# Optimization experiments

Measured on AMD Instinct MI355X. Metric: run time of the kernel, lower is better.

## Reference

```python
import jax, jax.numpy as jnp
import numpy as np

H = 256
W = 256
CHUNK = 100  # faces per rasterizer scan step


def _cross2(o, p, q):
    # 2D cross product of (p-o) x (q-o); broadcasts over leading dims
    return (p[..., 0] - o[..., 0]) * (q[..., 1] - o[..., 1]) - (p[..., 1] - o[..., 1]) * (q[..., 0] - o[..., 0])


def transform(verts, K, Rt):
    # verts [B,V,3] -> pixel coords [B,V,3] = (x_pix, y_pix, z_cam)
    v_cam = jnp.einsum('bij,bnj->bni', Rt[:, :, :3], verts) + Rt[:, None, :, 3]
    v_proj = jnp.einsum('bij,bnj->bni', K, v_cam)
    z = v_cam[..., 2:3]
    return jnp.concatenate([v_proj[..., :2] / z, z], axis=-1)


def _pixel_centers(h, w, dtype):
    px = jnp.arange(w, dtype=dtype) + 0.5
    py = jnp.arange(h, dtype=dtype) + 0.5
    gx, gy = jnp.meshgrid(px, py, indexing='xy')  # [h,w]
    return gx, gy


def rasterize(v_pix, vi, h, w):
    # z-buffered triangle rasterization -> index image [B,h,w] (int32, -1 = bg)
    B = v_pix.shape[0]
    Fc = vi.shape[0]
    gx, gy = _pixel_centers(h, w, v_pix.dtype)
    pix = jnp.stack([gx.ravel(), gy.ravel()], axis=-1)  # [HW,2]
    face_ids = jnp.arange(Fc, dtype=jnp.int32).reshape(-1, CHUNK)
    inf = jnp.asarray(jnp.inf, v_pix.dtype)

    def step(carry, fids):
        best_z, best_i = carry
        tri = vi[fids]                      # [C,3]
        p = v_pix[:, tri]                   # [B,C,3,3]
        a, b, c = p[:, :, 0], p[:, :, 1], p[:, :, 2]
        area = _cross2(a[..., :2], b[..., :2], c[..., :2])  # [B,C]
        pixb = pix[None, None]              # [1,1,HW,2]
        w0 = _cross2(b[..., None, :2], c[..., None, :2], pixb)  # [B,C,HW]
        w1 = _cross2(c[..., None, :2], a[..., None, :2], pixb)
        w2 = _cross2(a[..., None, :2], b[..., None, :2], pixb)
        s = jnp.sign(area)[..., None]
        nz = jnp.abs(area)[..., None] > 1e-8
        inside = (w0 * s >= 0) & (w1 * s >= 0) & (w2 * s >= 0) & nz
        za, zb, zc = a[..., 2:3], b[..., 2:3], c[..., 2:3]
        valid = inside & (za > 0) & (zb > 0) & (zc > 0)
        ar = jnp.where(jnp.abs(area) > 1e-8, area, 1.0)[..., None]
        invz = (w0 / ar) / za + (w1 / ar) / zb + (w2 / ar) / zc  # persp-correct 1/z
        z = jnp.where(valid & (invz > 0), 1.0 / jnp.maximum(invz, 1e-12), inf)
        cz = z.min(axis=1)                  # [B,HW]
        ci = z.argmin(axis=1)
        cf = fids[ci]
        upd = cz < best_z
        return (jnp.where(upd, cz, best_z), jnp.where(upd, cf, best_i)), None

    init = (jnp.full((B, h * w), jnp.inf, v_pix.dtype), jnp.full((B, h * w), -1, jnp.int32))
    (_, bi), _ = jax.lax.scan(step, init, face_ids)
    return bi.reshape(B, h, w)


def render(v_pix, vi, index_img):
    # depth [B,h,w] and perspective-correct barycentrics [B,3,h,w]
    B, h, w = index_img.shape
    tri = vi[jnp.clip(index_img, 0)]                 # [B,h,w,3]
    p = jax.vmap(lambda v, t: v[t])(v_pix, tri)      # [B,h,w,3,3]
    gx, gy = _pixel_centers(h, w, v_pix.dtype)
    pt = jnp.stack([gx, gy], axis=-1)[None]          # [1,h,w,2]
    a, b, c = p[..., 0, :], p[..., 1, :], p[..., 2, :]
    w0 = _cross2(b[..., :2], c[..., :2], pt)
    w1 = _cross2(c[..., :2], a[..., :2], pt)
    w2 = _cross2(a[..., :2], b[..., :2], pt)
    area = w0 + w1 + w2
    ar = jnp.where(jnp.abs(area) > 1e-8, area, 1.0)
    f0 = (w0 / ar) / jnp.maximum(a[..., 2], 1e-8)
    f1 = (w1 / ar) / jnp.maximum(b[..., 2], 1e-8)
    f2 = (w2 / ar) / jnp.maximum(c[..., 2], 1e-8)
    invz = f0 + f1 + f2
    invz_s = jnp.where(jnp.abs(invz) > 1e-12, invz, 1.0)
    depth = 1.0 / invz_s
    bary = jnp.stack([f0, f1, f2], axis=-1) / invz_s[..., None]  # [B,h,w,3]
    m = index_img != -1
    depth_img = jnp.where(m, depth, 0.0)
    bary_img = jnp.where(m[..., None], bary, 0.0).transpose(0, 3, 1, 2)  # [B,3,h,w]
    return depth_img, bary_img


def interpolate(attr, vti, index_img, bary_img):
    # attr [B,N,D], bary_img [B,3,h,w] -> [B,D,h,w]
    tri = vti[jnp.clip(index_img, 0)]                # [B,h,w,3]
    av = jax.vmap(lambda a, t: a[t])(attr, tri)      # [B,h,w,3,D]
    return jnp.einsum('bhwkd,bkhw->bdhw', av, bary_img)


def grid_sample_bilinear(tex, grid):
    # tex [B,C,Ht,Wt], grid [B,h,w,2] in [-1,1]; align_corners=False, zero pad
    B, C, Ht, Wt = tex.shape
    x = (grid[..., 0] + 1.0) * Wt / 2.0 - 0.5
    y = (grid[..., 1] + 1.0) * Ht / 2.0 - 0.5
    x0 = jnp.floor(x)
    y0 = jnp.floor(y)
    wx = (x - x0)[:, None]
    wy = (y - y0)[:, None]
    x0i = x0.astype(jnp.int32)
    y0i = y0.astype(jnp.int32)

    def gat(ix, iy):
        valid = (ix >= 0) & (ix < Wt) & (iy >= 0) & (iy < Ht)
        ixc = jnp.clip(ix, 0, Wt - 1)
        iyc = jnp.clip(iy, 0, Ht - 1)
        v = jax.vmap(lambda t, yy, xx: t[:, yy, xx])(tex, iyc, ixc)  # [B,C,h,w]
        return v * valid[:, None].astype(tex.dtype)

    return (gat(x0i, y0i) * (1 - wx) * (1 - wy)
            + gat(x0i + 1, y0i) * wx * (1 - wy)
            + gat(x0i, y0i + 1) * (1 - wx) * wy
            + gat(x0i + 1, y0i + 1) * wx * wy)


def reference(verts, tex, K, Rt, vt, vi, vti):
    v_pix = transform(verts, K, Rt)
    index_img = jax.lax.stop_gradient(rasterize(v_pix, vi, H, W))
    depth_img, bary_img = render(v_pix, vi, index_img)
    B = verts.shape[0]
    vt_attr = jnp.broadcast_to((vt * 2.0 - 1.0)[None], (B,) + vt.shape)
    vt_img = interpolate(vt_attr, vti, index_img, bary_img)    # [B,2,H,W]
    mask = (index_img != -1)[:, None].astype(tex.dtype)
    img = grid_sample_bilinear(tex, vt_img.transpose(0, 2, 3, 1)) * mask
    # edge_grad_estimator is identity in the forward pass
    return img, depth_img, v_pix, vt_img, index_img, bary_img, mask


def setup_inputs() -> dict:
    key = jax.random.key(0)
    ks = jax.random.split(key, 6)
    B, V, Fc, Nvt = 2, 5000, 10000, 5000
    xy = jax.random.uniform(ks[0], (B, V, 2), minval=-1.5, maxval=1.5)
    z = jax.random.uniform(ks[1], (B, V, 1), minval=2.0, maxval=4.0)
    verts = jnp.concatenate([xy, z], axis=-1)
    tex = jax.random.uniform(ks[2], (B, 3, 1024, 1024), dtype=jnp.float32)
    K = jnp.broadcast_to(jnp.array([[256., 0., 128.], [0., 256., 128.], [0., 0., 1.]], dtype=jnp.float32), (B, 3, 3))
    Rt = jnp.broadcast_to(jnp.concatenate([jnp.eye(3, dtype=jnp.float32), jnp.zeros((3, 1), jnp.float32)], axis=1), (B, 3, 4))
    vt = jax.random.uniform(ks[3], (Nvt, 2), dtype=jnp.float32)
    vi = jax.random.randint(ks[4], (Fc, 3), 0, V).astype(jnp.int32)
    vti = jax.random.randint(ks[5], (Fc, 3), 0, Nvt).astype(jnp.int32)
    return {"verts": verts, "tex": tex, "K": K, "Rt": Rt, "vt": vt, "vi": vi, "vti": vti}
```

## Files before the change

### kernel.cpp

```cpp
#include <hip/hip_runtime.h>
#include <cmath>

#define H_ 256
#define W_ 256
#define NB 256
#define BANDSH 3
#define NBAND (H_ >> BANDSH)
#define ILV 4
#define INITKEY 0x7f800000FFFFFFFFull

__device__ inline unsigned fkey(float f) {
  unsigned u = __float_as_uint(f);
  return (u & 0x80000000u) ? ~u : (u | 0x80000000u);
}
__device__ inline float unfkey(unsigned k) {
  return (k & 0x80000000u) ? __uint_as_float(k & 0x7fffffffu) : __uint_as_float(~k);
}

__device__ inline int zbucket(float zmin, float zlo, float scale) {
  int bkt = 0;
  if (zmin == zmin) bkt = min(NB - 1, max(0, (int)((zmin - zlo) * scale)));
  return bkt;
}

__global__ void k_transform(const float* __restrict__ verts, const float* __restrict__ Km,
                            const float* __restrict__ Rt, float* __restrict__ vpix,
                            int B, int V) {
  int i = blockIdx.x * blockDim.x + threadIdx.x;
  if (i >= B * V) return;
  int b = i / V;
  float x = verts[(size_t)i * 3 + 0], y = verts[(size_t)i * 3 + 1], z = verts[(size_t)i * 3 + 2];
  const float* R = Rt + (size_t)b * 12;
  float cx = __fadd_rn(__fadd_rn(__fadd_rn(__fmul_rn(R[0], x), __fmul_rn(R[1], y)), __fmul_rn(R[2], z)), R[3]);
  float cy = __fadd_rn(__fadd_rn(__fadd_rn(__fmul_rn(R[4], x), __fmul_rn(R[5], y)), __fmul_rn(R[6], z)), R[7]);
  float cz = __fadd_rn(__fadd_rn(__fadd_rn(__fmul_rn(R[8], x), __fmul_rn(R[9], y)), __fmul_rn(R[10], z)), R[11]);
  const float* Kb = Km + (size_t)b * 9;
  float px = __fadd_rn(__fadd_rn(__fmul_rn(Kb[0], cx), __fmul_rn(Kb[1], cy)), __fmul_rn(Kb[2], cz));
  float py = __fadd_rn(__fadd_rn(__fmul_rn(Kb[3], cx), __fmul_rn(Kb[4], cy)), __fmul_rn(Kb[5], cz));
  vpix[(size_t)i * 3 + 0] = __fdiv_rn(px, cz);
  vpix[(size_t)i * 3 + 1] = __fdiv_rn(py, cz);
  vpix[(size_t)i * 3 + 2] = cz;
}

__global__ void k_init(int* __restrict__ cnt, int* __restrict__ bcur, int n,
                       unsigned* __restrict__ minmax) {
  int i = blockIdx.x * blockDim.x + threadIdx.x;
  if (i < n) { cnt[i] = 0; bcur[i] = 0; }
  if (i == 0) { minmax[0] = 0xFFFFFFFFu; minmax[1] = 0u; }
}

__global__ void k_faceprep(const float* __restrict__ vpix, const int* __restrict__ vi,
                           float4* __restrict__ sA, float4* __restrict__ sB4,
                           float4* __restrict__ sC, float4* __restrict__ sZ1,
                           float4* __restrict__ meta, unsigned* __restrict__ minmax,
                           int B, int V, int F) {
  int i = blockIdx.x * blockDim.x + threadIdx.x;
  unsigned kmin = 0xFFFFFFFFu, kmax = 0u;
  if (i < B * F) {
    int b = i / F, f = i - b * F;
    int i0 = vi[f * 3 + 0], i1 = vi[f * 3 + 1], i2 = vi[f * 3 + 2];
    const float* base = vpix + (size_t)b * V * 3;
    float ax = base[(size_t)i0 * 3], ay = base[(size_t)i0 * 3 + 1], az = base[(size_t)i0 * 3 + 2];
    float bx = base[(size_t)i1 * 3], by = base[(size_t)i1 * 3 + 1], bz = base[(size_t)i1 * 3 + 2];
    float cx = base[(size_t)i2 * 3], cy = base[(size_t)i2 * 3 + 1], cz = base[(size_t)i2 * 3 + 2];
    float e0x = __fsub_rn(cx, bx), e0y = __fsub_rn(cy, by);
    float e1x = __fsub_rn(ax, cx), e1y = __fsub_rn(ay, cy);
    float e2x = __fsub_rn(bx, ax), e2y = __fsub_rn(by, ay);
    float area = __fsub_rn(__fmul_rn(e2x, __fsub_rn(cy, ay)), __fmul_rn(e2y, __fsub_rn(cx, ax)));
    float s = (area > 0.f) ? 1.f : ((area < 0.f) ? -1.f : 0.f);
    bool nz = fabsf(area) > 1e-8f;
    bool zv = (az > 0.f) && (bz > 0.f) && (cz > 0.f);
    float sp = (nz && zv) ? s : __uint_as_float(0x7fc00000u);
    float ar = nz ? area : 1.0f;
    float zmin = fminf(az, fminf(bz, cz));
    sA[i]  = make_float4(ax, ay, bx, by);
    sB4[i] = make_float4(cx, cy, __fmul_rn(sp, e0x), __fmul_rn(sp, e0y));
    sC[i]  = make_float4(__fmul_rn(sp, e1x), __fmul_rn(sp, e1y),
                         __fmul_rn(sp, e2x), __fmul_rn(sp, e2y));
    sZ1[i] = make_float4(az, bz, cz, __fmul_rn(sp, ar));
    unsigned bbox = 0x00000001u;
    if (sp == sp) {
      float minx = fminf(ax, fminf(bx, cx)), maxx = fmaxf(ax, fmaxf(bx, cx));
      float miny = fminf(ay, fminf(by, cy)), maxy = fmaxf(ay, fmaxf(by, cy));
      int xl = (int)ceilf(fmaxf(fminf(minx - 0.5f, 1e9f), -1e9f));
      int xh = (int)floorf(fmaxf(fminf(maxx - 0.5f, 1e9f), -1e9f));
      int yl = (int)ceilf(fmaxf(fminf(miny - 0.5f, 1e9f), -1e9f));
      int yh = (int)floorf(fmaxf(fminf(maxy - 0.5f, 1e9f), -1e9f));
      if (!(xl > xh || yl > yh || xh < 0 || xl > W_ - 1 || yh < 0 || yl > H_ - 1)) {
        int xlo = max(xl, 0), xhi = min(xh, W_ - 1);
        int ylo = max(yl, 0), yhi = min(yh, H_ - 1);
        bbox = (unsigned)xlo | ((unsigned)xhi << 8) | ((unsigned)ylo << 16) | ((unsigned)yhi << 24);
      }
    }
    meta[i] = make_float4(zmin, __uint_as_float(bbox), 0.f, 0.f);
    if (zmin == zmin) { kmin = fkey(zmin); kmax = kmin; }
  }
  #pragma unroll
  for (int m = 32; m >= 1; m >>= 1) {
    kmin = min(kmin, (unsigned)__shfl_xor((int)kmin, m));
    kmax = max(kmax, (unsigned)__shfl_xor((int)kmax, m));
  }
  if ((threadIdx.x & 63) == 0) {
    atomicMin(&minmax[0], kmin);
    atomicMax(&minmax[1], kmax);
  }
}

__global__ void k_hist(const float4* __restrict__ meta, const unsigned* __restrict__ minmax,
                       int* __restrict__ cnt, int B, int F) {
  int i = blockIdx.x * blockDim.x + threadIdx.x;
  if (i >= B * F) return;
  int b = i / F;
  float4 m = meta[i];
  unsigned bbox = __float_as_uint(m.y);
  int xlo = (int)(bbox & 255u), xhi = (int)((bbox >> 8) & 255u);
  if (xlo > xhi) return;
  float zlo = unfkey(minmax[0]), zhi = unfkey(minmax[1]);
  float scale = (float)NB / fmaxf(zhi - zlo, 1e-12f);
  int bkt = zbucket(m.x, zlo, scale);
  int ylo = (int)((bbox >> 16) & 255u), yhi = (int)(bbox >> 24);
  for (int band = (ylo >> BANDSH); band <= (yhi >> BANDSH); ++band)
    atomicAdd(&cnt[(b * NBAND + band) * NB + bkt], 1);
}

__global__ void k_bandscan(const int* __restrict__ cnt, int* __restrict__ bstart) {
  __shared__ int sh[NB];
  int rowi = blockIdx.x;
  int t = threadIdx.x;
  sh[t] = cnt[rowi * NB + t];
  __syncthreads();
  int self = sh[t];
  for (int ofs = 1; ofs < NB; ofs <<= 1) {
    int u = (t >= ofs) ? sh[t - ofs] : 0;
    __syncthreads();
    sh[t] += u;
    __syncthreads();
  }
  bstart[rowi * (NB + 1) + t] = sh[t] - self;
  if (t == NB - 1) bstart[rowi * (NB + 1) + NB] = sh[t];
}

__global__ void k_scatter(const float4* __restrict__ meta, const unsigned* __restrict__ minmax,
                          const int* __restrict__ bstart, int* __restrict__ bcur,
                          uint4* __restrict__ list, int B, int F) {
  int i = blockIdx.x * blockDim.x + threadIdx.x;
  if (i >= B * F) return;
  int b = i / F, f = i - b * F;
  float4 m = meta[i];
  unsigned bbox = __float_as_uint(m.y);
  int xlo = (int)(bbox & 255u), xhi = (int)((bbox >> 8) & 255u);
  if (xlo > xhi) return;
  float zlo = unfkey(minmax[0]), zhi = unfkey(minmax[1]);
  float rng = fmaxf(zhi - zlo, 1e-12f);
  float scale = (float)NB / rng;
  int bkt = zbucket(m.x, zlo, scale);
  float floorval = zlo + (float)bkt * (rng / (float)NB);
  uint4 ent = make_uint4(bbox, (unsigned)f, __float_as_uint(m.x), __float_as_uint(floorval));
  int ylo = (int)((bbox >> 16) & 255u), yhi = (int)(bbox >> 24);
  for (int band = (ylo >> BANDSH); band <= (yhi >> BANDSH); ++band) {
    int rowi = b * NBAND + band;
    int slot = bstart[rowi * (NB + 1) + bkt] + atomicAdd(&bcur[rowi * NB + bkt], 1);
    list[(size_t)rowi * F + slot] = ent;
  }
}

__global__ __launch_bounds__(64 * ILV) void k_raster_band(const uint4* __restrict__ list,
                                                          const int* __restrict__ bstart,
                                                          const float4* __restrict__ sA,
                                                          const float4* __restrict__ sB4,
                                                          const float4* __restrict__ sC,
                                                          const float4* __restrict__ sZ1,
                                                          float* __restrict__ o_idx,
                                                          int B, int F) {
  int seg = blockIdx.x;
  int y   = blockIdx.y;
  int b   = blockIdx.z;
  int tid = threadIdx.x;
  int w = tid >> 6, lane = tid & 63;
  __shared__ unsigned long long sk[64];
  if (tid < 64) sk[tid] = INITKEY;
  __syncthreads();
  int rowi = b * NBAND + (y >> BANDSH);
  int len = bstart[rowi * (NB + 1) + NB];
  const uint4* L = list + (size_t)rowi * F;
  size_t fb = (size_t)b * F;
  float px = seg * 64 + lane + 0.5f, py = y + 0.5f;
  int sx0 = seg * 64, sx1 = sx0 + 63;
  unsigned long long bestkey = INITKEY;
  float bestz = INFINITY;
  int it = 0;
  int pos = w;
  uint4 e = (pos < len) ? L[pos] : make_uint4(0x00000001u, 0u, 0u, 0x7f800000u);
  while (pos < len) {
    int nxt = pos + ILV;
    uint4 en = L[(nxt < len) ? nxt : (len - 1)];
    float floor0 = __fmul_rn(__uint_as_float(e.w), 0.9999f) - 1e-5f;
    if (__all(floor0 > bestz)) break;
    ++it;
    if ((it & 7) == 0) {
      unsigned long long old = atomicMin(&sk[lane], bestkey);
      if (old < bestkey) { bestkey = old; bestz = __uint_as_float((unsigned)(bestkey >> 32)); }
    }
    int xlo = (int)(e.x & 255u), xhi = (int)((e.x >> 8) & 255u);
    int ylo = (int)((e.x >> 16) & 255u), yhi = (int)(e.x >> 24);
    bool cull = (y < ylo) || (y > yhi) || (xhi < sx0) || (xlo > sx1);
    if (!cull) {
      int f = (int)e.y;
      float4 a0 = sA[fb + f];
      float4 a1 = sB4[fb + f];
      float4 a2 = sC[fb + f];
      float t0 = __fsub_rn(__fmul_rn(a1.z, __fsub_rn(py, a0.w)), __fmul_rn(a1.w, __fsub_rn(px, a0.z)));
      float t1 = __fsub_rn(__fmul_rn(a2.x, __fsub_rn(py, a1.y)), __fmul_rn(a2.y, __fsub_rn(px, a1.x)));
      float t2 = __fsub_rn(__fmul_rn(a2.z, __fsub_rn(py, a0.y)), __fmul_rn(a2.w, __fsub_rn(px, a0.x)));
      bool inside = (t0 >= 0.f) && (t1 >= 0.f) && (t2 >= 0.f);
      if (inside && !(__fmul_rn(__uint_as_float(e.z), 0.9999f) > bestz)) {
        float4 zz = sZ1[fb + f];
        float u0 = __fdiv_rn(__fdiv_rn(t0, zz.w), zz.x);
        float u1 = __fdiv_rn(__fdiv_rn(t1, zz.w), zz.y);
        float u2 = __fdiv_rn(__fdiv_rn(t2, zz.w), zz.z);
        float invz = __fadd_rn(__fadd_rn(u0, u1), u2);
        if (invz > 0.f) {
          float z = __fdiv_rn(1.0f, fmaxf(invz, 1e-12f));
          unsigned long long ck = ((unsigned long long)__float_as_uint(z) << 32) | e.y;
          if (ck < bestkey) {
            bestkey = ck; bestz = z;
            atomicMin(&sk[lane], ck);
          }
        }
      }
    }
    pos = nxt;
    e = en;
  }
  atomicMin(&sk[lane], bestkey);
  __syncthreads();
  if (tid < 64) {
    unsigned long long k = sk[tid];
    unsigned zb = (unsigned)(k >> 32);
    o_idx[(size_t)b * (H_ * W_) + (size_t)y * W_ + seg * 64 + tid] =
        (zb >= 0x7f800000u) ? -1.0f : (float)(int)(unsigned)(k & 0xffffffffu);
  }
}

__global__ void k_raster_direct(const float* __restrict__ vpix, const int* __restrict__ vi,
                                float* __restrict__ idxout, int B, int V, int F) {
  int p = blockIdx.x * blockDim.x + threadIdx.x;
  if (p >= B * H_ * W_) return;
  int b = p / (H_ * W_); int pid = p - b * (H_ * W_);
  float px = (pid & (W_ - 1)) + 0.5f, py = (pid >> 8) + 0.5f;
  const float* base = vpix + (size_t)b * V * 3;
  float bestz = INFINITY; int besti = -1;
  for (int f = 0; f < F; ++f) {
    int i0 = vi[f * 3], i1 = vi[f * 3 + 1], i2 = vi[f * 3 + 2];
    float ax = base[(size_t)i0 * 3], ay = base[(size_t)i0 * 3 + 1], za = base[(size_t)i0 * 3 + 2];
    float bx = base[(size_t)i1 * 3], by = base[(size_t)i1 * 3 + 1], zb = base[(size_t)i1 * 3 + 2];
    float cx = base[(size_t)i2 * 3], cy = base[(size_t)i2 * 3 + 1], zc = base[(size_t)i2 * 3 + 2];
    float e0x = __fsub_rn(cx, bx), e0y = __fsub_rn(cy, by);
    float e1x = __fsub_rn(ax, cx), e1y = __fsub_rn(ay, cy);
    float e2x = __fsub_rn(bx, ax), e2y = __fsub_rn(by, ay);
    float area = __fsub_rn(__fmul_rn(e2x, __fsub_rn(cy, ay)), __fmul_rn(e2y, __fsub_rn(cx, ax)));
    float s = (area > 0.f) ? 1.f : ((area < 0.f) ? -1.f : 0.f);
    bool nz = fabsf(area) > 1e-8f;
    bool zv = (za > 0.f) && (zb > 0.f) && (zc > 0.f);
    float sp = (nz && zv) ? s : __uint_as_float(0x7fc00000u);
    float ar = nz ? area : 1.0f;
    float w0 = __fsub_rn(__fmul_rn(e0x, __fsub_rn(py, by)), __fmul_rn(e0y, __fsub_rn(px, bx)));
    float w1 = __fsub_rn(__fmul_rn(e1x, __fsub_rn(py, cy)), __fmul_rn(e1y, __fsub_rn(px, cx)));
    float w2 = __fsub_rn(__fmul_rn(e2x, __fsub_rn(py, ay)), __fmul_rn(e2y, __fsub_rn(px, ax)));
    bool inside = (__fmul_rn(w0, sp) >= 0.f) && (__fmul_rn(w1, sp) >= 0.f) && (__fmul_rn(w2, sp) >= 0.f);
    if (inside) {
      float invz = __fadd_rn(__fadd_rn(__fdiv_rn(__fdiv_rn(w0, ar), za),
                                       __fdiv_rn(__fdiv_rn(w1, ar), zb)),
                             __fdiv_rn(__fdiv_rn(w2, ar), zc));
      if (invz > 0.f) {
        float z = __fdiv_rn(1.0f, fmaxf(invz, 1e-12f));
        if (z < bestz) { bestz = z; besti = f; }
      }
    }
  }
  idxout[p] = (float)besti;
}

__global__ __launch_bounds__(256) void k_render(const float* __restrict__ vpix, const int* __restrict__ vi,
                                                const int* __restrict__ vti, const float* __restrict__ vt,
                                                const float* __restrict__ tex, const float* __restrict__ idxin,
                                                float* __restrict__ o_img, float* __restrict__ o_depth,
                                                float* __restrict__ o_vt, float* __restrict__ o_bary,
                                                float* __restrict__ o_mask,
                                                int B, int V, int F, int TH, int TW) {
  int p = blockIdx.x * blockDim.x + threadIdx.x;
  if (p >= B * H_ * W_) return;
  int HW = H_ * W_;
  int b = p / HW; int pid = p - b * HW;
  int y = pid >> 8, x = pid & (W_ - 1);
  int idx = (int)idxin[p];
  size_t pix2 = (size_t)b * 2 * HW + pid;
  size_t pix3 = (size_t)b * 3 * HW + pid;
  if (idx < 0) {
    o_depth[p] = 0.f; o_mask[p] = 0.f;
    o_vt[pix2] = 0.f; o_vt[pix2 + HW] = 0.f;
    o_bary[pix3] = 0.f; o_bary[pix3 + HW] = 0.f; o_bary[pix3 + 2 * HW] = 0.f;
    o_img[pix3] = 0.f; o_img[pix3 + HW] = 0.f; o_img[pix3 + 2 * HW] = 0.f;
    return;
  }
  const float* base = vpix + (size_t)b * V * 3;
  int i0 = vi[idx * 3], i1 = vi[idx * 3 + 1], i2 = vi[idx * 3 + 2];
  float ax = base[(size_t)i0 * 3], ay = base[(size_t)i0 * 3 + 1], az = base[(size_t)i0 * 3 + 2];
  float bx = base[(size_t)i1 * 3], by = base[(size_t)i1 * 3 + 1], bz = base[(size_t)i1 * 3 + 2];
  float cx = base[(size_t)i2 * 3], cy = base[(size_t)i2 * 3 + 1], cz = base[(size_t)i2 * 3 + 2];
  float ptx = x + 0.5f, pty = y + 0.5f;
  float w0 = __fsub_rn(__fmul_rn(__fsub_rn(cx, bx), __fsub_rn(pty, by)),
                       __fmul_rn(__fsub_rn(cy, by), __fsub_rn(ptx, bx)));
  float w1 = __fsub_rn(__fmul_rn(__fsub_rn(ax, cx), __fsub_rn(pty, cy)),
                       __fmul_rn(__fsub_rn(ay, cy), __fsub_rn(ptx, cx)));
  float w2 = __fsub_rn(__fmul_rn(__fsub_rn(bx, ax), __fsub_rn(pty, ay)),
                       __fmul_rn(__fsub_rn(by, ay), __fsub_rn(ptx, ax)));
  float area = __fadd_rn(__fadd_rn(w0, w1), w2);
  float ar = (fabsf(area) > 1e-8f) ? area : 1.0f;
  float f0 = __fdiv_rn(__fdiv_rn(w0, ar), fmaxf(az, 1e-8f));
  float f1 = __fdiv_rn(__fdiv_rn(w1, ar), fmaxf(bz, 1e-8f));
  float f2 = __fdiv_rn(__fdiv_rn(w2, ar), fmaxf(cz, 1e-8f));
  float invz = __fadd_rn(__fadd_rn(f0, f1), f2);
  float invz_s = (fabsf(invz) > 1e-12f) ? invz : 1.0f;
  float depth = __fdiv_rn(1.0f, invz_s);
  float bary0 = __fdiv_rn(f0, invz_s);
  float bary1 = __fdiv_rn(f1, invz_s);
  float bary2 = __fdiv_rn(f2, invz_s);
  o_depth[p] = depth; o_mask[p] = 1.0f;
  o_bary[pix3] = bary0; o_bary[pix3 + HW] = bary1; o_bary[pix3 + 2 * HW] = bary2;
  int t0 = vti[idx * 3], t1 = vti[idx * 3 + 1], t2 = vti[idx * 3 + 2];
  float u0x = __fsub_rn(__fmul_rn(vt[(size_t)t0 * 2], 2.f), 1.f);
  float u0y = __fsub_rn(__fmul_rn(vt[(size_t)t0 * 2 + 1], 2.f), 1.f);
  float u1x = __fsub_rn(__fmul_rn(vt[(size_t)t1 * 2], 2.f), 1.f);
  float u1y = __fsub_rn(__fmul_rn(vt[(size_t)t1 * 2 + 1], 2.f), 1.f);
  float u2x = __fsub_rn(__fmul_rn(vt[(size_t)t2 * 2], 2.f), 1.f);
  float u2y = __fsub_rn(__fmul_rn(vt[(size_t)t2 * 2 + 1], 2.f), 1.f);
  float gx = __fadd_rn(__fadd_rn(__fmul_rn(u0x, bary0), __fmul_rn(u1x, bary1)), __fmul_rn(u2x, bary2));
  float gy = __fadd_rn(__fadd_rn(__fmul_rn(u0y, bary0), __fmul_rn(u1y, bary1)), __fmul_rn(u2y, bary2));
  o_vt[pix2] = gx; o_vt[pix2 + HW] = gy;
  float sx = __fsub_rn(__fdiv_rn(__fmul_rn(__fadd_rn(gx, 1.0f), (float)TW), 2.0f), 0.5f);
  float sy = __fsub_rn(__fdiv_rn(__fmul_rn(__fadd_rn(gy, 1.0f), (float)TH), 2.0f), 0.5f);
  float x0f = floorf(sx), y0f = floorf(sy);
  float wx = __fsub_rn(sx, x0f), wy = __fsub_rn(sy, y0f);
  float omx = __fsub_rn(1.0f, wx), omy = __fsub_rn(1.0f, wy);
  int x0 = (int)x0f, y0 = (int)y0f;
  int x1 = x0 + 1, y1 = y0 + 1;
  bool v00 = (x0 >= 0) && (x0 < TW) && (y0 >= 0) && (y0 < TH);
  bool v10 = (x1 >= 0) && (x1 < TW) && (y0 >= 0) && (y0 < TH);
  bool v01 = (x0 >= 0) && (x0 < TW) && (y1 >= 0) && (y1 < TH);
  bool v11 = (x1 >= 0) && (x1 < TW) && (y1 >= 0) && (y1 < TH);
  int x0c = min(max(x0, 0), TW - 1), x1c = min(max(x1, 0), TW - 1);
  int y0c = min(max(y0, 0), TH - 1), y1c = min(max(y1, 0), TH - 1);
  const float* tb = tex + (size_t)b * 3 * TH * TW;
  #pragma unroll
  for (int ch = 0; ch < 3; ++ch) {
    const float* tc = tb + (size_t)ch * TH * TW;
    float g00 = v00 ? tc[(size_t)y0c * TW + x0c] : 0.f;
    float g10 = v10 ? tc[(size_t)y0c * TW + x1c] : 0.f;
    float g01 = v01 ? tc[(size_t)y1c * TW + x0c] : 0.f;
    float g11 = v11 ? tc[(size_t)y1c * TW + x1c] : 0.f;
    float r = __fmul_rn(__fmul_rn(g00, omx), omy);
    r = __fadd_rn(r, __fmul_rn(__fmul_rn(g10, wx), omy));
    r = __fadd_rn(r, __fmul_rn(__fmul_rn(g01, omx), wy));
    r = __fadd_rn(r, __fmul_rn(__fmul_rn(g11, wx), wy));
    o_img[pix3 + (size_t)ch * HW] = r;
  }
}

extern "C" void kernel_launch(void* const* d_in, const int* in_sizes, int n_in,
                              void* d_out, int out_size, void* d_ws, size_t ws_size,
                              hipStream_t stream) {
  const float* verts = (const float*)d_in[0];
  const float* tex   = (const float*)d_in[1];
  const float* Km    = (const float*)d_in[2];
  const float* Rt    = (const float*)d_in[3];
  const float* vt    = (const float*)d_in[4];
  const int*   vi    = (const int*)d_in[5];
  const int*   vti   = (const int*)d_in[6];

  int B = in_sizes[2] / 9;
  int V = in_sizes[0] / (3 * B);
  int F = in_sizes[5] / 3;
  long texhw = (long)in_sizes[1] / (B * 3);
  int TH = (int)(sqrt((double)texhw) + 0.5);
  int TW = TH;
  const int HW = H_ * W_;

  float* out = (float*)d_out;
  float* o_img   = out;
  float* o_depth = o_img + (size_t)B * 3 * HW;
  float* o_vpix  = o_depth + (size_t)B * HW;
  float* o_vt    = o_vpix + (size_t)B * V * 3;
  float* o_idx   = o_vt + (size_t)B * 2 * HW;
  float* o_bary  = o_idx + (size_t)B * HW;
  float* o_mask  = o_bary + (size_t)B * 3 * HW;

  k_transform<<<(B * V + 255) / 256, 256, 0, stream>>>(verts, Km, Rt, o_vpix, B, V);

  size_t f4Bytes   = (size_t)B * F * 16;
  size_t listBytes = (size_t)B * NBAND * F * 16;
  size_t cntBytes  = (size_t)B * NBAND * NB * 4;
  size_t bstBytes  = (size_t)B * NBAND * (NB + 1) * 4;
  size_t need = 5 * f4Bytes + listBytes + 2 * cntBytes + bstBytes + 64;

  if (ws_size >= need) {
    char* w = (char*)d_ws;
    float4* sA   = (float4*)w;  w += f4Bytes;
    float4* sB4  = (float4*)w;  w += f4Bytes;
    float4* sC   = (float4*)w;  w += f4Bytes;
    float4* sZ1  = (float4*)w;  w += f4Bytes;
    float4* meta = (float4*)w;  w += f4Bytes;
    uint4*  list = (uint4*)w;   w += listBytes;
    int*    cnt  = (int*)w;     w += cntBytes;
    int*    bcur = (int*)w;     w += cntBytes;
    int*    bst  = (int*)w;     w += bstBytes;
    unsigned* minmax = (unsigned*)w;

    int ninit = B * NBAND * NB;
    k_init<<<(ninit + 255) / 256, 256, 0, stream>>>(cnt, bcur, ninit, minmax);
    k_faceprep<<<(B * F + 255) / 256, 256, 0, stream>>>(o_vpix, vi, sA, sB4, sC, sZ1,
                                                        meta, minmax, B, V, F);
    k_hist<<<(B * F + 255) / 256, 256, 0, stream>>>(meta, minmax, cnt, B, F);
    k_bandscan<<<B * NBAND, NB, 0, stream>>>(cnt, bst);
    k_scatter<<<(B * F + 255) / 256, 256, 0, stream>>>(meta, minmax, bst, bcur, list, B, F);
    dim3 rg(W_ / 64, H_, B);
    k_raster_band<<<rg, 64 * ILV, 0, stream>>>(list, bst, sA, sB4, sC, sZ1, o_idx, B, F);
  } else {
    k_raster_direct<<<(B * HW + 255) / 256, 256, 0, stream>>>(o_vpix, vi, o_idx, B, V, F);
  }

  k_render<<<(B * HW + 255) / 256, 256, 0, stream>>>(o_vpix, vi, vti, vt, tex, o_idx,
                                                     o_img, o_depth, o_vt, o_bary, o_mask,
                                                     B, V, F, TH, TW);
}
```

Measured before the change: 380.6 us.

## Fuse z-range into transform, histogram into faceprep, add precomputed-record render

The depth range reduction moves into the vertex transform kernel, and the bucket histogram is folded into face preparation. This removes the separate histogram pass and the recomputation of buckets in scatter. The raster loop broadcasts list entries with readfirstlane and culls using a 64-pixel segment mask instead of a full x-bbox. A new render kernel reads per-face edge and UV records prepared in faceprep rather than re-gathering vertices, at the cost of four extra per-face float4 arrays of workspace. The z range is now taken over all vertices rather than face minima, which changes bucket boundaries.

```diff
diff --git a/kernel.cpp b/kernel.cpp
--- a/kernel.cpp
+++ b/kernel.cpp
@@ -25,21 +25,35 @@
 
 __global__ void k_transform(const float* __restrict__ verts, const float* __restrict__ Km,
                             const float* __restrict__ Rt, float* __restrict__ vpix,
-                            int B, int V) {
+                            unsigned* __restrict__ minmax, int B, int V) {
   int i = blockIdx.x * blockDim.x + threadIdx.x;
-  if (i >= B * V) return;
-  int b = i / V;
-  float x = verts[(size_t)i * 3 + 0], y = verts[(size_t)i * 3 + 1], z = verts[(size_t)i * 3 + 2];
-  const float* R = Rt + (size_t)b * 12;
-  float cx = __fadd_rn(__fadd_rn(__fadd_rn(__fmul_rn(R[0], x), __fmul_rn(R[1], y)), __fmul_rn(R[2], z)), R[3]);
-  float cy = __fadd_rn(__fadd_rn(__fadd_rn(__fmul_rn(R[4], x), __fmul_rn(R[5], y)), __fmul_rn(R[6], z)), R[7]);
-  float cz = __fadd_rn(__fadd_rn(__fadd_rn(__fmul_rn(R[8], x), __fmul_rn(R[9], y)), __fmul_rn(R[10], z)), R[11]);
-  const float* Kb = Km + (size_t)b * 9;
-  float px = __fadd_rn(__fadd_rn(__fmul_rn(Kb[0], cx), __fmul_rn(Kb[1], cy)), __fmul_rn(Kb[2], cz));
-  float py = __fadd_rn(__fadd_rn(__fmul_rn(Kb[3], cx), __fmul_rn(Kb[4], cy)), __fmul_rn(Kb[5], cz));
-  vpix[(size_t)i * 3 + 0] = __fdiv_rn(px, cz);
-  vpix[(size_t)i * 3 + 1] = __fdiv_rn(py, cz);
-  vpix[(size_t)i * 3 + 2] = cz;
+  unsigned kmin = 0xFFFFFFFFu, kmax = 0u;
+  if (i < B * V) {
+    int b = i / V;
+    float x = verts[(size_t)i * 3 + 0], y = verts[(size_t)i * 3 + 1], z = verts[(size_t)i * 3 + 2];
+    const float* R = Rt + (size_t)b * 12;
+    float cx = __fadd_rn(__fadd_rn(__fadd_rn(__fmul_rn(R[0], x), __fmul_rn(R[1], y)), __fmul_rn(R[2], z)), R[3]);
+    float cy = __fadd_rn(__fadd_rn(__fadd_rn(__fmul_rn(R[4], x), __fmul_rn(R[5], y)), __fmul_rn(R[6], z)), R[7]);
+    float cz = __fadd_rn(__fadd_rn(__fadd_rn(__fmul_rn(R[8], x), __fmul_rn(R[9], y)), __fmul_rn(R[10], z)), R[11]);
+    const float* Kb = Km + (size_t)b * 9;
+    float px = __fadd_rn(__fadd_rn(__fmul_rn(Kb[0], cx), __fmul_rn(Kb[1], cy)), __fmul_rn(Kb[2], cz));
+    float py = __fadd_rn(__fadd_rn(__fmul_rn(Kb[3], cx), __fmul_rn(Kb[4], cy)), __fmul_rn(Kb[5], cz));
+    vpix[(size_t)i * 3 + 0] = __fdiv_rn(px, cz);
+    vpix[(size_t)i * 3 + 1] = __fdiv_rn(py, cz);
+    vpix[(size_t)i * 3 + 2] = cz;
+    if (minmax && cz == cz) { kmin = fkey(cz); kmax = kmin; }
+  }
+  if (minmax) {
+    #pragma unroll
+    for (int m = 32; m >= 1; m >>= 1) {
+      kmin = min(kmin, (unsigned)__shfl_xor((int)kmin, m));
+      kmax = max(kmax, (unsigned)__shfl_xor((int)kmax, m));
+    }
+    if ((threadIdx.x & 63) == 0) {
+      atomicMin(&minmax[0], kmin);
+      atomicMax(&minmax[1], kmax);
+    }
+  }
 }
 
 __global__ void k_init(int* __restrict__ cnt, int* __restrict__ bcur, int n,
@@ -50,77 +64,71 @@
 }
 
 __global__ void k_faceprep(const float* __restrict__ vpix, const int* __restrict__ vi,
+                           const int* __restrict__ vti, const float* __restrict__ vt,
                            float4* __restrict__ sA, float4* __restrict__ sB4,
                            float4* __restrict__ sC, float4* __restrict__ sZ1,
-                           float4* __restrict__ meta, unsigned* __restrict__ minmax,
-                           int B, int V, int F) {
-  int i = blockIdx.x * blockDim.x + threadIdx.x;
-  unsigned kmin = 0xFFFFFFFFu, kmax = 0u;
-  if (i < B * F) {
-    int b = i / F, f = i - b * F;
-    int i0 = vi[f * 3 + 0], i1 = vi[f * 3 + 1], i2 = vi[f * 3 + 2];
-    const float* base = vpix + (size_t)b * V * 3;
-    float ax = base[(size_t)i0 * 3], ay = base[(size_t)i0 * 3 + 1], az = base[(size_t)i0 * 3 + 2];
-    float bx = base[(size_t)i1 * 3], by = base[(size_t)i1 * 3 + 1], bz = base[(size_t)i1 * 3 + 2];
-    float cx = base[(size_t)i2 * 3], cy = base[(size_t)i2 * 3 + 1], cz = base[(size_t)i2 * 3 + 2];
-    float e0x = __fsub_rn(cx, bx), e0y = __fsub_rn(cy, by);
-    float e1x = __fsub_rn(ax, cx), e1y = __fsub_rn(ay, cy);
-    float e2x = __fsub_rn(bx, ax), e2y = __fsub_rn(by, ay);
-    float area = __fsub_rn(__fmul_rn(e2x, __fsub_rn(cy, ay)), __fmul_rn(e2y, __fsub_rn(cx, ax)));
-    float s = (area > 0.f) ? 1.f : ((area < 0.f) ? -1.f : 0.f);
-    bool nz = fabsf(area) > 1e-8f;
-    bool zv = (az > 0.f) && (bz > 0.f) && (cz > 0.f);
-    float sp = (nz && zv) ? s : __uint_as_float(0x7fc00000u);
-    float ar = nz ? area : 1.0f;
-    float zmin = fminf(az, fminf(bz, cz));
-    sA[i]  = make_float4(ax, ay, bx, by);
-    sB4[i] = make_float4(cx, cy, __fmul_rn(sp, e0x), __fmul_rn(sp, e0y));
-    sC[i]  = make_float4(__fmul_rn(sp, e1x), __fmul_rn(sp, e1y),
-                         __fmul_rn(sp, e2x), __fmul_rn(sp, e2y));
-    sZ1[i] = make_float4(az, bz, cz, __fmul_rn(sp, ar));
-    unsigned bbox = 0x00000001u;
-    if (sp == sp) {
-      float minx = fminf(ax, fminf(bx, cx)), maxx = fmaxf(ax, fmaxf(bx, cx));
-      float miny = fminf(ay, fminf(by, cy)), maxy = fmaxf(ay, fmaxf(by, cy));
-      int xl = (int)ceilf(fmaxf(fminf(minx - 0.5f, 1e9f), -1e9f));
-      int xh = (int)floorf(fmaxf(fminf(maxx - 0.5f, 1e9f), -1e9f));
-      int yl = (int)ceilf(fmaxf(fminf(miny - 0.5f, 1e9f), -1e9f));
-      int yh = (int)floorf(fmaxf(fminf(maxy - 0.5f, 1e9f), -1e9f));
-      if (!(xl > xh || yl > yh || xh < 0 || xl > W_ - 1 || yh < 0 || yl > H_ - 1)) {
-        int xlo = max(xl, 0), xhi = min(xh, W_ - 1);
-        int ylo = max(yl, 0), yhi = min(yh, H_ - 1);
-        bbox = (unsigned)xlo | ((unsigned)xhi << 8) | ((unsigned)ylo << 16) | ((unsigned)yhi << 24);
-      }
-    }
-    meta[i] = make_float4(zmin, __uint_as_float(bbox), 0.f, 0.f);
-    if (zmin == zmin) { kmin = fkey(zmin); kmax = kmin; }
-  }
-  #pragma unroll
-  for (int m = 32; m >= 1; m >>= 1) {
-    kmin = min(kmin, (unsigned)__shfl_xor((int)kmin, m));
-    kmax = max(kmax, (unsigned)__shfl_xor((int)kmax, m));
-  }
-  if ((threadIdx.x & 63) == 0) {
-    atomicMin(&minmax[0], kmin);
-    atomicMax(&minmax[1], kmax);
-  }
-}
-
-__global__ void k_hist(const float4* __restrict__ meta, const unsigned* __restrict__ minmax,
-                       int* __restrict__ cnt, int B, int F) {
+                           float4* __restrict__ sE1, float4* __restrict__ sE2,
+                           float4* __restrict__ sUV12, float4* __restrict__ sUV2,
+                           float4* __restrict__ meta, const unsigned* __restrict__ minmax,
+                           int* __restrict__ cnt, int B, int V, int F) {
   int i = blockIdx.x * blockDim.x + threadIdx.x;
   if (i >= B * F) return;
-  int b = i / F;
-  float4 m = meta[i];
-  unsigned bbox = __float_as_uint(m.y);
-  int xlo = (int)(bbox & 255u), xhi = (int)((bbox >> 8) & 255u);
-  if (xlo > xhi) return;
+  int b = i / F, f = i - b * F;
+  int i0 = vi[f * 3 + 0], i1 = vi[f * 3 + 1], i2 = vi[f * 3 + 2];
+  const float* base = vpix + (size_t)b * V * 3;
+  float ax = base[(size_t)i0 * 3], ay = base[(size_t)i0 * 3 + 1], az = base[(size_t)i0 * 3 + 2];
+  float bx = base[(size_t)i1 * 3], by = base[(size_t)i1 * 3 + 1], bz = base[(size_t)i1 * 3 + 2];
+  float cx = base[(size_t)i2 * 3], cy = base[(size_t)i2 * 3 + 1], cz = base[(size_t)i2 * 3 + 2];
+  float e0x = __fsub_rn(cx, bx), e0y = __fsub_rn(cy, by);
+  float e1x = __fsub_rn(ax, cx), e1y = __fsub_rn(ay, cy);
+  float e2x = __fsub_rn(bx, ax), e2y = __fsub_rn(by, ay);
+  float area = __fsub_rn(__fmul_rn(e2x, __fsub_rn(cy, ay)), __fmul_rn(e2y, __fsub_rn(cx, ax)));
+  float s = (area > 0.f) ? 1.f : ((area < 0.f) ? -1.f : 0.f);
+  bool nz = fabsf(area) > 1e-8f;
+  bool zv = (az > 0.f) && (bz > 0.f) && (cz > 0.f);
+  float sp = (nz && zv) ? s : __uint_as_float(0x7fc00000u);
+  float ar = nz ? area : 1.0f;
+  float zmin = fminf(az, fminf(bz, cz));
+  sA[i]  = make_float4(ax, ay, bx, by);
+  sB4[i] = make_float4(cx, cy, __fmul_rn(sp, e0x), __fmul_rn(sp, e0y));
+  sC[i]  = make_float4(__fmul_rn(sp, e1x), __fmul_rn(sp, e1y),
+                       __fmul_rn(sp, e2x), __fmul_rn(sp, e2y));
+  sZ1[i] = make_float4(az, bz, cz, __fmul_rn(sp, ar));
+  sE1[i] = make_float4(cx, cy, e0x, e0y);
+  sE2[i] = make_float4(e1x, e1y, e2x, e2y);
+  int t0 = vti[f * 3], t1 = vti[f * 3 + 1], t2 = vti[f * 3 + 2];
+  float u0x = __fsub_rn(__fmul_rn(vt[(size_t)t0 * 2], 2.f), 1.f);
+  float u0y = __fsub_rn(__fmul_rn(vt[(size_t)t0 * 2 + 1], 2.f), 1.f);
+  float u1x = __fsub_rn(__fmul_rn(vt[(size_t)t1 * 2], 2.f), 1.f);
+  float u1y = __fsub_rn(__fmul_rn(vt[(size_t)t1 * 2 + 1], 2.f), 1.f);
+  float u2x = __fsub_rn(__fmul_rn(vt[(size_t)t2 * 2], 2.f), 1.f);
+  float u2y = __fsub_rn(__fmul_rn(vt[(size_t)t2 * 2 + 1], 2.f), 1.f);
+  sUV12[i] = make_float4(u0x, u0y, u1x, u1y);
+  sUV2[i]  = make_float4(u2x, u2y, 0.f, 0.f);
+  unsigned pack = 0u;
+  int bkt = 0; float floorval = 0.f;
   float zlo = unfkey(minmax[0]), zhi = unfkey(minmax[1]);
-  float scale = (float)NB / fmaxf(zhi - zlo, 1e-12f);
-  int bkt = zbucket(m.x, zlo, scale);
-  int ylo = (int)((bbox >> 16) & 255u), yhi = (int)(bbox >> 24);
-  for (int band = (ylo >> BANDSH); band <= (yhi >> BANDSH); ++band)
-    atomicAdd(&cnt[(b * NBAND + band) * NB + bkt], 1);
+  float rng = fmaxf(zhi - zlo, 1e-12f);
+  float scale = (float)NB / rng;
+  if (sp == sp) {
+    float minx = fminf(ax, fminf(bx, cx)), maxx = fmaxf(ax, fmaxf(bx, cx));
+    float miny = fminf(ay, fminf(by, cy)), maxy = fmaxf(ay, fmaxf(by, cy));
+    int xl = (int)ceilf(fmaxf(fminf(minx - 0.5f, 1e9f), -1e9f));
+    int xh = (int)floorf(fmaxf(fminf(maxx - 0.5f, 1e9f), -1e9f));
+    int yl = (int)ceilf(fmaxf(fminf(miny - 0.5f, 1e9f), -1e9f));
+    int yh = (int)floorf(fmaxf(fminf(maxy - 0.5f, 1e9f), -1e9f));
+    if (!(xl > xh || yl > yh || xh < 0 || xl > W_ - 1 || yh < 0 || yl > H_ - 1)) {
+      int xlo = max(xl, 0), xhi = min(xh, W_ - 1);
+      int ylo = max(yl, 0), yhi = min(yh, H_ - 1);
+      unsigned segmask = (((1u << ((xhi >> 6) + 1)) - 1u) & ~((1u << (xlo >> 6)) - 1u)) & 0xFu;
+      pack = segmask | ((unsigned)ylo << 8) | ((unsigned)yhi << 16);
+      bkt = zbucket(zmin, zlo, scale);
+      floorval = zlo + (float)bkt * (rng / (float)NB);
+      for (int band = (ylo >> BANDSH); band <= (yhi >> BANDSH); ++band)
+        atomicAdd(&cnt[(b * NBAND + band) * NB + bkt], 1);
+    }
+  }
+  meta[i] = make_float4(zmin, __uint_as_float(pack), __int_as_float(bkt), floorval);
 }
 
 __global__ void k_bandscan(const int* __restrict__ cnt, int* __restrict__ bstart) {
@@ -140,23 +148,18 @@
   if (t == NB - 1) bstart[rowi * (NB + 1) + NB] = sh[t];
 }
 
-__global__ void k_scatter(const float4* __restrict__ meta, const unsigned* __restrict__ minmax,
+__global__ void k_scatter(const float4* __restrict__ meta,
                           const int* __restrict__ bstart, int* __restrict__ bcur,
                           uint4* __restrict__ list, int B, int F) {
   int i = blockIdx.x * blockDim.x + threadIdx.x;
   if (i >= B * F) return;
   int b = i / F, f = i - b * F;
   float4 m = meta[i];
-  unsigned bbox = __float_as_uint(m.y);
-  int xlo = (int)(bbox & 255u), xhi = (int)((bbox >> 8) & 255u);
-  if (xlo > xhi) return;
-  float zlo = unfkey(minmax[0]), zhi = unfkey(minmax[1]);
-  float rng = fmaxf(zhi - zlo, 1e-12f);
-  float scale = (float)NB / rng;
-  int bkt = zbucket(m.x, zlo, scale);
-  float floorval = zlo + (float)bkt * (rng / (float)NB);
-  uint4 ent = make_uint4(bbox, (unsigned)f, __float_as_uint(m.x), __float_as_uint(floorval));
-  int ylo = (int)((bbox >> 16) & 255u), yhi = (int)(bbox >> 24);
+  unsigned pack = __float_as_uint(m.y);
+  if ((pack & 0xFu) == 0u) return;
+  int bkt = __float_as_int(m.z);
+  uint4 ent = make_uint4(pack, (unsigned)f, __float_as_uint(m.x), __float_as_uint(m.w));
+  int ylo = (int)((pack >> 8) & 255u), yhi = (int)((pack >> 16) & 255u);
   for (int band = (ylo >> BANDSH); band <= (yhi >> BANDSH); ++band) {
     int rowi = b * NBAND + band;
     int slot = bstart[rowi * (NB + 1) + bkt] + atomicAdd(&bcur[rowi * NB + bkt], 1);
@@ -185,43 +188,44 @@
   const uint4* L = list + (size_t)rowi * F;
   size_t fb = (size_t)b * F;
   float px = seg * 64 + lane + 0.5f, py = y + 0.5f;
-  int sx0 = seg * 64, sx1 = sx0 + 63;
   unsigned long long bestkey = INITKEY;
   float bestz = INFINITY;
   int it = 0;
   int pos = w;
-  uint4 e = (pos < len) ? L[pos] : make_uint4(0x00000001u, 0u, 0u, 0x7f800000u);
+  uint4 e = (pos < len) ? L[pos] : make_uint4(0u, 0u, 0u, 0x7f800000u);
   while (pos < len) {
     int nxt = pos + ILV;
     uint4 en = L[(nxt < len) ? nxt : (len - 1)];
-    float floor0 = __fmul_rn(__uint_as_float(e.w), 0.9999f) - 1e-5f;
+    unsigned pack = __builtin_amdgcn_readfirstlane(e.x);
+    int      fid  = __builtin_amdgcn_readfirstlane((int)e.y);
+    float    zmn  = __uint_as_float(__builtin_amdgcn_readfirstlane(e.z));
+    float    zfl  = __uint_as_float(__builtin_amdgcn_readfirstlane(e.w));
+    float floor0 = __fmul_rn(zfl, 0.9999f) - 1e-5f;
     if (__all(floor0 > bestz)) break;
     ++it;
     if ((it & 7) == 0) {
       unsigned long long old = atomicMin(&sk[lane], bestkey);
       if (old < bestkey) { bestkey = old; bestz = __uint_as_float((unsigned)(bestkey >> 32)); }
     }
-    int xlo = (int)(e.x & 255u), xhi = (int)((e.x >> 8) & 255u);
-    int ylo = (int)((e.x >> 16) & 255u), yhi = (int)(e.x >> 24);
-    bool cull = (y < ylo) || (y > yhi) || (xhi < sx0) || (xlo > sx1);
+    bool cull = !((pack >> seg) & 1u) ||
+                (y < (int)((pack >> 8) & 255u)) || (y > (int)((pack >> 16) & 255u));
     if (!cull) {
-      int f = (int)e.y;
-      float4 a0 = sA[fb + f];
-      float4 a1 = sB4[fb + f];
-      float4 a2 = sC[fb + f];
+      float4 a0 = sA[fb + fid];
+      float4 a1 = sB4[fb + fid];
+      float4 a2 = sC[fb + fid];
       float t0 = __fsub_rn(__fmul_rn(a1.z, __fsub_rn(py, a0.w)), __fmul_rn(a1.w, __fsub_rn(px, a0.z)));
       float t1 = __fsub_rn(__fmul_rn(a2.x, __fsub_rn(py, a1.y)), __fmul_rn(a2.y, __fsub_rn(px, a1.x)));
       float t2 = __fsub_rn(__fmul_rn(a2.z, __fsub_rn(py, a0.y)), __fmul_rn(a2.w, __fsub_rn(px, a0.x)));
       bool inside = (t0 >= 0.f) && (t1 >= 0.f) && (t2 >= 0.f);
-      if (inside && !(__fmul_rn(__uint_as_float(e.z), 0.9999f) > bestz)) {
-        float4 zz = sZ1[fb + f];
+      if (inside && !(__fmul_rn(zmn, 0.9999f) > bestz)) {
+        float4 zz = sZ1[fb + fid];
         float u0 = __fdiv_rn(__fdiv_rn(t0, zz.w), zz.x);
         float u1 = __fdiv_rn(__fdiv_rn(t1, zz.w), zz.y);
         float u2 = __fdiv_rn(__fdiv_rn(t2, zz.w), zz.z);
         float invz = __fadd_rn(__fadd_rn(u0, u1), u2);
         if (invz > 0.f) {
           float z = __fdiv_rn(1.0f, fmaxf(invz, 1e-12f));
-          unsigned long long ck = ((unsigned long long)__float_as_uint(z) << 32) | e.y;
+          unsigned long long ck = ((unsigned long long)__float_as_uint(z) << 32) | (unsigned)fid;
           if (ck < bestkey) {
             bestkey = ck; bestz = z;
             atomicMin(&sk[lane], ck);
@@ -279,6 +283,89 @@
     }
   }
   idxout[p] = (float)besti;
+}
+
+__global__ __launch_bounds__(256) void k_render_rec(const float4* __restrict__ sA,
+                                                    const float4* __restrict__ sE1,
+                                                    const float4* __restrict__ sE2,
+                                                    const float4* __restrict__ sZ1,
+                                                    const float4* __restrict__ sUV12,
+                                                    const float4* __restrict__ sUV2,
+                                                    const float* __restrict__ tex,
+                                                    const float* __restrict__ idxin,
+                                                    float* __restrict__ o_img, float* __restrict__ o_depth,
+                                                    float* __restrict__ o_vt, float* __restrict__ o_bary,
+                                                    float* __restrict__ o_mask,
+                                                    int B, int F, int TH, int TW) {
+  int p = blockIdx.x * blockDim.x + threadIdx.x;
+  if (p >= B * H_ * W_) return;
+  int HW = H_ * W_;
+  int b = p / HW; int pid = p - b * HW;
+  int y = pid >> 8, x = pid & (W_ - 1);
+  int idx = (int)idxin[p];
+  size_t pix2 = (size_t)b * 2 * HW + pid;
+  size_t pix3 = (size_t)b * 3 * HW + pid;
+  if (idx < 0) {
+    o_depth[p] = 0.f; o_mask[p] = 0.f;
+    o_vt[pix2] = 0.f; o_vt[pix2 + HW] = 0.f;
+    o_bary[pix3] = 0.f; o_bary[pix3 + HW] = 0.f; o_bary[pix3 + 2 * HW] = 0.f;
+    o_img[pix3] = 0.f; o_img[pix3 + HW] = 0.f; o_img[pix3 + 2 * HW] = 0.f;
+    return;
+  }
+  size_t gp = (size_t)b * F + idx;
+  float4 a0 = sA[gp];
+  float4 e1 = sE1[gp];
+  float4 e2 = sE2[gp];
+  float4 zz = sZ1[gp];
+  float4 uv = sUV12[gp];
+  float4 uv2 = sUV2[gp];
+  float ptx = x + 0.5f, pty = y + 0.5f;
+  float w0 = __fsub_rn(__fmul_rn(e1.z, __fsub_rn(pty, a0.w)), __fmul_rn(e1.w, __fsub_rn(ptx, a0.z)));
+  float w1 = __fsub_rn(__fmul_rn(e2.x, __fsub_rn(pty, e1.y)), __fmul_rn(e2.y, __fsub_rn(ptx, e1.x)));
+  float w2 = __fsub_rn(__fmul_rn(e2.z, __fsub_rn(pty, a0.y)), __fmul_rn(e2.w, __fsub_rn(ptx, a0.x)));
+  float area = __fadd_rn(__fadd_rn(w0, w1), w2);
+  float ar = (fabsf(area) > 1e-8f) ? area : 1.0f;
+  float f0 = __fdiv_rn(__fdiv_rn(w0, ar), fmaxf(zz.x, 1e-8f));
+  float f1 = __fdiv_rn(__fdiv_rn(w1, ar), fmaxf(zz.y, 1e-8f));
+  float f2 = __fdiv_rn(__fdiv_rn(w2, ar), fmaxf(zz.z, 1e-8f));
+  float invz = __fadd_rn(__fadd_rn(f0, f1), f2);
+  float invz_s = (fabsf(invz) > 1e-12f) ? invz : 1.0f;
+  float depth = __fdiv_rn(1.0f, invz_s);
+  float bary0 = __fdiv_rn(f0, invz_s);
+  float bary1 = __fdiv_rn(f1, invz_s);
+  float bary2 = __fdiv_rn(f2, invz_s);
+  o_depth[p] = depth; o_mask[p] = 1.0f;
+  o_bary[pix3] = bary0; o_bary[pix3 + HW] = bary1; o_bary[pix3 + 2 * HW] = bary2;
+  float gx = __fadd_rn(__fadd_rn(__fmul_rn(uv.x, bary0), __fmul_rn(uv.z, bary1)), __fmul_rn(uv2.x, bary2));
+  float gy = __fadd_rn(__fadd_rn(__fmul_rn(uv.y, bary0), __fmul_rn(uv.w, bary1)), __fmul_rn(uv2.y, bary2));
+  o_vt[pix2] = gx; o_vt[pix2 + HW] = gy;
+  float sx = __fsub_rn(__fdiv_rn(__fmul_rn(__fadd_rn(gx, 1.0f), (float)TW), 2.0f), 0.5f);
+  float sy = __fsub_rn(__fdiv_rn(__fmul_rn(__fadd_rn(gy, 1.0f), (float)TH), 2.0f), 0.5f);
+  float x0f = floorf(sx), y0f = floorf(sy);
+  float wx = __fsub_rn(sx, x0f), wy = __fsub_rn(sy, y0f);
+  float omx = __fsub_rn(1.0f, wx), omy = __fsub_rn(1.0f, wy);
+  int x0 = (int)x0f, y0 = (int)y0f;
+  int x1 = x0 + 1, y1 = y0 + 1;
+  bool v00 = (x0 >= 0) && (x0 < TW) && (y0 >= 0) && (y0 < TH);
+  bool v10 = (x1 >= 0) && (x1 < TW) && (y0 >= 0) && (y0 < TH);
+  bool v01 = (x0 >= 0) && (x0 < TW) && (y1 >= 0) && (y1 < TH);
+  bool v11 = (x1 >= 0) && (x1 < TW) && (y1 >= 0) && (y1 < TH);
+  int x0c = min(max(x0, 0), TW - 1), x1c = min(max(x1, 0), TW - 1);
+  int y0c = min(max(y0, 0), TH - 1), y1c = min(max(y1, 0), TH - 1);
+  const float* tb = tex + (size_t)b * 3 * TH * TW;
+  #pragma unroll
+  for (int ch = 0; ch < 3; ++ch) {
+    const float* tc = tb + (size_t)ch * TH * TW;
+    float g00 = v00 ? tc[(size_t)y0c * TW + x0c] : 0.f;
+    float g10 = v10 ? tc[(size_t)y0c * TW + x1c] : 0.f;
+    float g01 = v01 ? tc[(size_t)y1c * TW + x0c] : 0.f;
+    float g11 = v11 ? tc[(size_t)y1c * TW + x1c] : 0.f;
+    float r = __fmul_rn(__fmul_rn(g00, omx), omy);
+    r = __fadd_rn(r, __fmul_rn(__fmul_rn(g10, wx), omy));
+    r = __fadd_rn(r, __fmul_rn(__fmul_rn(g01, omx), wy));
+    r = __fadd_rn(r, __fmul_rn(__fmul_rn(g11, wx), wy));
+    o_img[pix3 + (size_t)ch * HW] = r;
+  }
 }
 
 __global__ __launch_bounds__(256) void k_render(const float* __restrict__ vpix, const int* __restrict__ vi,
@@ -395,41 +482,49 @@
   float* o_bary  = o_idx + (size_t)B * HW;
   float* o_mask  = o_bary + (size_t)B * 3 * HW;
 
-  k_transform<<<(B * V + 255) / 256, 256, 0, stream>>>(verts, Km, Rt, o_vpix, B, V);
-
   size_t f4Bytes   = (size_t)B * F * 16;
   size_t listBytes = (size_t)B * NBAND * F * 16;
   size_t cntBytes  = (size_t)B * NBAND * NB * 4;
   size_t bstBytes  = (size_t)B * NBAND * (NB + 1) * 4;
-  size_t need = 5 * f4Bytes + listBytes + 2 * cntBytes + bstBytes + 64;
+  size_t need = 9 * f4Bytes + listBytes + 2 * cntBytes + bstBytes + 64;
 
   if (ws_size >= need) {
     char* w = (char*)d_ws;
-    float4* sA   = (float4*)w;  w += f4Bytes;
-    float4* sB4  = (float4*)w;  w += f4Bytes;
-    float4* sC   = (float4*)w;  w += f4Bytes;
-    float4* sZ1  = (float4*)w;  w += f4Bytes;
-    float4* meta = (float4*)w;  w += f4Bytes;
-    uint4*  list = (uint4*)w;   w += listBytes;
-    int*    cnt  = (int*)w;     w += cntBytes;
-    int*    bcur = (int*)w;     w += cntBytes;
-    int*    bst  = (int*)w;     w += bstBytes;
+    float4* sA    = (float4*)w;  w += f4Bytes;
+    float4* sB4   = (float4*)w;  w += f4Bytes;
+    float4* sC    = (float4*)w;  w += f4Bytes;
+    float4* sZ1   = (float4*)w;  w += f4Bytes;
+    float4* sE1   = (float4*)w;  w += f4Bytes;
+    float4* sE2   = (float4*)w;  w += f4Bytes;
+    float4* sUV12 = (float4*)w;  w += f4Bytes;
+    float4* sUV2  = (float4*)w;  w += f4Bytes;
+    float4* meta  = (float4*)w;  w += f4Bytes;
+    uint4*  list  = (uint4*)w;   w += listBytes;
+    int*    cnt   = (int*)w;     w += cntBytes;
+    int*    bcur  = (int*)w;     w += cntBytes;
+    int*    bst   = (int*)w;     w += bstBytes;
     unsigned* minmax = (unsigned*)w;
 
     int ninit = B * NBAND * NB;
     k_init<<<(ninit + 255) / 256, 256, 0, stream>>>(cnt, bcur, ninit, minmax);
-    k_faceprep<<<(B * F + 255) / 256, 256, 0, stream>>>(o_vpix, vi, sA, sB4, sC, sZ1,
-                                                        meta, minmax, B, V, F);
-    k_hist<<<(B * F + 255) / 256, 256, 0, stream>>>(meta, minmax, cnt, B, F);
+    k_transform<<<(B * V + 255) / 256, 256, 0, stream>>>(verts, Km, Rt, o_vpix, minmax, B, V);
+    k_faceprep<<<(B * F + 255) / 256, 256, 0, stream>>>(o_vpix, vi, vti, vt,
+                                                        sA, sB4, sC, sZ1, sE1, sE2, sUV12, sUV2,
+                                                        meta, minmax, cnt, B, V, F);
     k_bandscan<<<B * NBAND, NB, 0, stream>>>(cnt, bst);
-    k_scatter<<<(B * F + 255) / 256, 256, 0, stream>>>(meta, minmax, bst, bcur, list, B, F);
+    k_scatter<<<(B * F + 255) / 256, 256, 0, stream>>>(meta, bst, bcur, list, B, F);
     dim3 rg(W_ / 64, H_, B);
     k_raster_band<<<rg, 64 * ILV, 0, stream>>>(list, bst, sA, sB4, sC, sZ1, o_idx, B, F);
+    k_render_rec<<<(B * HW + 255) / 256, 256, 0, stream>>>(sA, sE1, sE2, sZ1, sUV12, sUV2,
+                                                           tex, o_idx,
+                                                           o_img, o_depth, o_vt, o_bary, o_mask,
+                                                           B, F, TH, TW);
   } else {
+    k_transform<<<(B * V + 255) / 256, 256, 0, stream>>>(verts, Km, Rt, o_vpix,
+                                                         (unsigned*)nullptr, B, V);
     k_raster_direct<<<(B * HW + 255) / 256, 256, 0, stream>>>(o_vpix, vi, o_idx, B, V, F);
-  }
-
-  k_render<<<(B * HW + 255) / 256, 256, 0, stream>>>(o_vpix, vi, vti, vt, tex, o_idx,
-                                                     o_img, o_depth, o_vt, o_bary, o_mask,
-                                                     B, V, F, TH, TW);
-}
+    k_render<<<(B * HW + 255) / 256, 256, 0, stream>>>(o_vpix, vi, vti, vt, tex, o_idx,
+                                                       o_img, o_depth, o_vt, o_bary, o_mask,
+                                                       B, V, F, TH, TW);
+  }
+}
```

Result: faster. 367.3 us (median of 3 runs) (-3.5%).
